# Optimization experiments

Measured on AMD Instinct MI355X. Metric: run time of the kernel, lower is better.

The kernel has to match this reference:

```python
import jax, jax.numpy as jnp
import numpy as np

B, T, D = 16, 4096, 256
CODEBOOK_SIZE = 1024
COMMITMENT = 1.0


def setup_inputs() -> dict:
    key = jax.random.key(0)
    kx, kc = jax.random.split(key)
    x = jax.random.normal(kx, (B, T, D), dtype=jnp.float32)
    codebook = jax.random.normal(kc, (CODEBOOK_SIZE, D), dtype=jnp.float32)
    return {"x": x, "codebook": codebook}


def reference(x, codebook):
    # x: [B, T, D] continuous latents; codebook: [K, D]
    flat = x.reshape(-1, x.shape[-1])  # [N, D]
    # does not affect argmin but is kept for faithfulness to torch.cdist-style math)
    x_sq = jnp.sum(flat * flat, axis=1, keepdims=True)            # [N, 1]
    c_sq = jnp.sum(codebook * codebook, axis=1)                   # [K]
    dist = x_sq - 2.0 * (flat @ codebook.T) + c_sq[None, :]       # [N, K]
    indices = jnp.argmin(dist, axis=1)                            # [N] int
    quantized = codebook[indices].reshape(x.shape)                # gather, [B, T, D]
    # commitment loss: encoder pulled toward (stopped) codes
    commit_loss = COMMITMENT * jnp.mean(
        (x - jax.lax.stop_gradient(quantized)) ** 2
    )
    # straight-through estimator
    out = x + jax.lax.stop_gradient(quantized - x)
    return out, indices.reshape(x.shape[:-1]), commit_loss
```

## Files before the change

kernel.cpp:

```cpp
#include <hip/hip_runtime.h>

#define N_TOK 65536
#define DIM   256
#define KCODE 1024

#define NTHREADS 256
#define TM 128
#define TN 128
#define BK 32
#define NCHUNK 8
#define NSTAGE 24

#define REFINE_EPS 0.125f
#define TIE_THETA 1.0e-4

#define WS_CSQ_OFF   16
#define WS_IDX_OFF   2048
#define WS_PAIRS_OFF (WS_IDX_OFF + N_TOK)
#define WS_CBPK_OFF  (WS_PAIRS_OFF + N_TOK * NCHUNK * 4)

typedef float f32x4  __attribute__((ext_vector_type(4)));
typedef short bf16x8 __attribute__((ext_vector_type(8)));
typedef short s16x8  __attribute__((ext_vector_type(8)));

__global__ void zero_loss_kernel(float* ws) {
    if (threadIdx.x == 0) ws[0] = 0.0f;
}

__global__ void rowsq_np_kernel(const float* __restrict__ m,
                                float* __restrict__ out, int rows) {
#pragma clang fp contract(off)
    int row = blockIdx.x * 16 + (threadIdx.x >> 4);
    int l   = threadIdx.x & 15;
    if (row >= rows) return;
    int h = l >> 3;
    int j = l & 7;
    const float* p = m + (size_t)row * DIM + h * 128 + j;
    float v = p[0];
    float r = v * v;
#pragma unroll
    for (int i = 1; i < 16; ++i) {
        float w  = p[i * 8];
        float w2 = w * w;
        r = r + w2;
    }
    float t = r + __shfl_xor(r, 1);
    t = t + __shfl_xor(t, 2);
    t = t + __shfl_xor(t, 4);
    t = t + __shfl_xor(t, 8);
    if (l == 0) out[row] = t;
}

__device__ __forceinline__ void ins2(float d, int idx,
                                     float& d1, int& i1, float& d2, int& i2) {
    if (d < d1 || (d == d1 && idx < i1)) {
        d2 = d1; i2 = i1; d1 = d; i1 = idx;
    } else if ((d < d2 || (d == d2 && idx < i2)) && idx != i1) {
        d2 = d; i2 = idx;
    }
}

__device__ __forceinline__ void f2bf_split(float v, short& hi, short& lo) {
    unsigned u = __float_as_uint(v);
    unsigned r = (u + 0x7fffu + ((u >> 16) & 1u)) >> 16;
    hi = (short)r;
    float hf = __uint_as_float(r << 16);
    float lf = v - hf;
    unsigned u2 = __float_as_uint(lf);
    unsigned r2 = (u2 + 0x7fffu + ((u2 >> 16) & 1u)) >> 16;
    lo = (short)r2;
}

__global__ void pack_tiles_kernel(const float* __restrict__ src,
                                  unsigned short* __restrict__ dst,
                                  int total) {
    int tid = blockIdx.x * blockDim.x + threadIdx.x;
    if (tid >= total) return;
    int s   = tid & 3;
    int r   = (tid >> 2) & 127;
    int kc  = (tid >> 9) & 7;
    int g   = tid >> 12;
    int oct = s ^ ((r >> 1) & 3);

    const float4* xr = reinterpret_cast<const float4*>(
        src + ((size_t)(g * 128 + r)) * DIM + kc * 32 + oct * 8);
    float4 v0 = xr[0];
    float4 v1 = xr[1];

    float f[8] = {v0.x, v0.y, v0.z, v0.w, v1.x, v1.y, v1.z, v1.w};
    s16x8 hv, lv;
#pragma unroll
    for (int i = 0; i < 8; ++i) {
        short h, l;
        f2bf_split(f[i], h, l);
        hv[i] = h; lv[i] = l;
    }
    size_t base_hi = (((size_t)(g * 16 + kc) * 128 + r) << 5) + s * 8;
    size_t base_lo = (((size_t)(g * 16 + 8 + kc) * 128 + r) << 5) + s * 8;
    *reinterpret_cast<s16x8*>(dst + base_hi) = hv;
    *reinterpret_cast<s16x8*>(dst + base_lo) = lv;
}

__device__ __forceinline__ void gload_lds16(const unsigned short* g, unsigned short* lds) {
    __builtin_amdgcn_global_load_lds(
        (const __attribute__((address_space(1))) unsigned int*)g,
        (__attribute__((address_space(3))) unsigned int*)lds, 16, 0, 0);
}

__launch_bounds__(NTHREADS, 5)
__global__ void vq_main_kernel(const unsigned short* __restrict__ xpk,
                               const unsigned short* __restrict__ cbpk,
                               const float* __restrict__ csq,
                               float4* __restrict__ pairs) {
    __shared__ __align__(16) unsigned short shbuf[2][2 * TM * BK];

    const int tid  = threadIdx.x;
    const int w    = tid >> 6;
    const int wy   = w >> 1;
    const int wx   = w & 1;
    const int lane = tid & 63;
    const int lm   = lane & 15;
    const int q    = lane >> 4;

    const int bx     = blockIdx.x;
    const int jj     = bx >> 3;
    const int grp    = (bx & 7) + ((jj >> 3) << 3);
    const int cchunk = jj & 7;
    const int tok0   = grp * TM;
    const int code0  = cchunk * TN;

    float cs_reg[4];
#pragma unroll
    for (int ni = 0; ni < 4; ++ni)
        cs_reg[ni] = csq[code0 + wx * 64 + ni * 16 + lm];

    f32x4 acc[4][4];
#pragma unroll
    for (int mi = 0; mi < 4; ++mi)
#pragma unroll
        for (int ni = 0; ni < 4; ++ni)
            acc[mi][ni] = (f32x4){0.f, 0.f, 0.f, 0.f};

    int offA[4], offB[4];
#pragma unroll
    for (int mi = 0; mi < 4; ++mi) {
        int r = wy * 64 + mi * 16 + lm;
        offA[mi] = r * BK + ((q ^ ((r >> 1) & 3)) * 8);
    }
#pragma unroll
    for (int ni = 0; ni < 4; ++ni) {
        int r = wx * 64 + ni * 16 + lm;
        offB[ni] = TM * BK + r * BK + ((q ^ ((r >> 1) & 3)) * 8);
    }

    const int lsrc = w * 1024 + lane * 8;
    auto stage = [&](int p, int s) {
        const int seg = s >> 3;
        const int kc  = s & 7;
        const int pa  = (seg == 2) ? 8 : 0;
        const int pb  = (seg == 1) ? 8 : 0;
        const unsigned short* ga = xpk  + (((size_t)(grp    * 16 + pa + kc)) << 12) + lsrc;
        const unsigned short* gb = cbpk + (((size_t)(cchunk * 16 + pb + kc)) << 12) + lsrc;
        unsigned short* At = &shbuf[p][w * 1024];
        unsigned short* Bt = &shbuf[p][TM * BK + w * 1024];
        gload_lds16(ga,       At);
        gload_lds16(ga + 512, At + 512);
        gload_lds16(gb,       Bt);
        gload_lds16(gb + 512, Bt + 512);
    };

    stage(0, 0);
    __syncthreads();

    int p = 0;
#pragma unroll 1
    for (int s = 0; s < NSTAGE; ++s) {
        if (s < NSTAGE - 1) stage(p ^ 1, s + 1);

        const unsigned short* buf = &shbuf[p][0];
        bf16x8 af[4], bf[4];
#pragma unroll
        for (int mi = 0; mi < 4; ++mi)
            af[mi] = *reinterpret_cast<const bf16x8*>(buf + offA[mi]);
#pragma unroll
        for (int ni = 0; ni < 4; ++ni)
            bf[ni] = *reinterpret_cast<const bf16x8*>(buf + offB[ni]);
#pragma unroll
        for (int mi = 0; mi < 4; ++mi)
#pragma unroll
            for (int ni = 0; ni < 4; ++ni)
                acc[mi][ni] = __builtin_amdgcn_mfma_f32_16x16x32_bf16(
                    af[mi], bf[ni], acc[mi][ni], 0, 0, 0);

        __syncthreads();
        p ^= 1;
    }

    float4 (*pairs_sh)[2] = reinterpret_cast<float4(*)[2]>(&shbuf[0][0]);

#pragma unroll
    for (int mi = 0; mi < 4; ++mi) {
#pragma unroll
        for (int r = 0; r < 4; ++r) {
            int row_local = wy * 64 + mi * 16 + q * 4 + r;
            float l1 = 3.4e38f, l2 = 3.4e38f;
            int   j1 = 0x7fffffff, j2 = 0x7fffffff;
#pragma unroll
            for (int ni = 0; ni < 4; ++ni) {
                float d = cs_reg[ni] - 2.0f * acc[mi][ni][r];
                ins2(d, code0 + wx * 64 + ni * 16 + lm, l1, j1, l2, j2);
            }
#pragma unroll
            for (int m = 1; m < 16; m <<= 1) {
                float o1 = __shfl_xor(l1, m);
                int   p1 = __shfl_xor(j1, m);
                float o2 = __shfl_xor(l2, m);
                int   p2 = __shfl_xor(j2, m);
                ins2(o1, p1, l1, j1, l2, j2);
                ins2(o2, p2, l1, j1, l2, j2);
            }
            if (lm == 0) {
                float4 pr;
                pr.x = l1; pr.y = l2;
                pr.z = __int_as_float(j1); pr.w = __int_as_float(j2);
                pairs_sh[row_local][wx] = pr;
            }
        }
    }
    __syncthreads();
    if (tid < TM) {
        float4 pa = pairs_sh[tid][0];
        float4 pb = pairs_sh[tid][1];
        float d1 = pa.x, d2 = pa.y;
        int   i1 = __float_as_int(pa.z), i2 = __float_as_int(pa.w);
        ins2(pb.x, __float_as_int(pb.z), d1, i1, d2, i2);
        ins2(pb.y, __float_as_int(pb.w), d1, i1, d2, i2);
        float4 pr;
        pr.x = d1; pr.y = d2;
        pr.z = __int_as_float(i1); pr.w = __int_as_float(i2);
        pairs[(size_t)(tok0 + tid) * NCHUNK + cchunk] = pr;
    }
}

__global__ void merge_refine_kernel(const float* __restrict__ x,
                                    const float* __restrict__ cb,
                                    const float4* __restrict__ pairs,
                                    int* __restrict__ idx_out) {
    int t = blockIdx.x * 256 + threadIdx.x;
    if (t >= N_TOK) return;
    float4 p0 = pairs[(size_t)t * NCHUNK];
    float d1 = p0.x, d2 = p0.y;
    int   i1 = __float_as_int(p0.z), i2 = __float_as_int(p0.w);
#pragma unroll
    for (int c = 1; c < NCHUNK; ++c) {
        float4 p = pairs[(size_t)t * NCHUNK + c];
        ins2(p.x, __float_as_int(p.z), d1, i1, d2, i2);
        ins2(p.y, __float_as_int(p.w), d1, i1, d2, i2);
    }

    int pick = i1;
    if (d2 - d1 < REFINE_EPS) {
        const float* xr = x + (size_t)t * DIM;
        const float* c1 = cb + (size_t)i1 * DIM;
        const float* c2 = cb + (size_t)i2 * DIM;
        double sA = 0.0, dA = 0.0, sB = 0.0, dB = 0.0;
        for (int k = 0; k < DIM; ++k) {
            double xv = (double)xr[k];
            double a  = (double)c1[k];
            double b  = (double)c2[k];
            sA += a * a; dA += xv * a;
            sB += b * b; dB += xv * b;
        }
        double DA  = sA - 2.0 * dA;
        double DB  = sB - 2.0 * dB;
        double gap = DB - DA;
        if (gap > TIE_THETA)       pick = i1;
        else if (gap < -TIE_THETA) pick = i2;
        else                       pick = (i1 < i2) ? i1 : i2;
    }
    idx_out[t] = pick;
}

__launch_bounds__(NTHREADS)
__global__ void output_kernel(const float* __restrict__ x,
                              const float* __restrict__ cb,
                              const int* __restrict__ idx,
                              float* __restrict__ out_q,
                              float* __restrict__ out_idx,
                              float* __restrict__ loss_ws) {
    __shared__ int   sh_idx[TM];
    __shared__ float wsum[4];
    const int tid  = threadIdx.x;
    const int tok0 = blockIdx.x * TM;

    if (tid < TM) sh_idx[tid] = idx[tok0 + tid];
    __syncthreads();

    float lsum = 0.0f;
    for (int t = 0; t < TM; ++t) {
        int code = sh_idx[t];
        float qv = cb[(size_t)code * DIM + tid];
        float xv = x[(size_t)(tok0 + t) * DIM + tid];
        out_q[(size_t)(tok0 + t) * DIM + tid] = xv + (qv - xv);
        float df = xv - qv;
        lsum = fmaf(df, df, lsum);
    }
    if (tid < TM) out_idx[tok0 + tid] = (float)sh_idx[tid];

#pragma unroll
    for (int off = 1; off < 64; off <<= 1) lsum += __shfl_xor(lsum, off);
    if ((tid & 63) == 0) wsum[tid >> 6] = lsum;
    __syncthreads();
    if (tid == 0) atomicAdd(loss_ws, (wsum[0] + wsum[1]) + (wsum[2] + wsum[3]));
}

__global__ void finalize_kernel(const float* ws, float* out_loss) {
    if (threadIdx.x == 0) out_loss[0] = ws[0] * (1.0f / 16777216.0f);
}

extern "C" void kernel_launch(void* const* d_in, const int* in_sizes, int n_in,
                              void* d_out, int out_size, void* d_ws, size_t ws_size,
                              hipStream_t stream) {
    const float* x  = (const float*)d_in[0];
    const float* cb = (const float*)d_in[1];

    float* out      = (float*)d_out;
    float* out_q    = out;
    float* out_idx  = out + (size_t)N_TOK * DIM;
    float* out_loss = out_idx + N_TOK;

    float*  ws    = (float*)d_ws;
    float*  csq   = ws + WS_CSQ_OFF;
    int*    idx   = (int*)(ws + WS_IDX_OFF);
    float4* pairs = (float4*)(ws + WS_PAIRS_OFF);
    unsigned short* cbpk = (unsigned short*)(ws + WS_CBPK_OFF);
    unsigned short* xpk  = (unsigned short*)out_q;

    zero_loss_kernel<<<1, 64, 0, stream>>>(ws);
    rowsq_np_kernel<<<KCODE / 16, 256, 0, stream>>>(cb, csq, KCODE);
    pack_tiles_kernel<<<(N_TOK * 32) / 256, 256, 0, stream>>>(x, xpk, N_TOK * 32);
    pack_tiles_kernel<<<(KCODE * 32) / 256, 256, 0, stream>>>(cb, cbpk, KCODE * 32);
    vq_main_kernel<<<(N_TOK / TM) * NCHUNK, NTHREADS, 0, stream>>>(xpk, cbpk, csq, pairs);
    merge_refine_kernel<<<N_TOK / 256, 256, 0, stream>>>(x, cb, pairs, idx);
    output_kernel<<<N_TOK / TM, NTHREADS, 0, stream>>>(x, cb, idx, out_q, out_idx, ws);
    finalize_kernel<<<1, 64, 0, stream>>>(ws, out_loss);
}
```

Measured before the change: 803.3 us.

## Load MFMA fragments directly from global memory instead of staging through LDS

The LDS double-buffered pipeline using global_load_lds is removed. Each wave now reads its bf16 fragments straight from the pre-packed global tiles, with the k-loop fully unrolled and no per-stage barriers. The pack layout drops the XOR swizzle, and the pairs buffer becomes chunk-major so merge reads are coalesced. This gives up LDS reuse across the waves, so each fragment is fetched from global or L2 by two waves, and the lower launch bound allows more registers per thread in exchange for occupancy.

```diff
diff --git a/kernel.cpp b/kernel.cpp
--- a/kernel.cpp
+++ b/kernel.cpp
@@ -7,7 +7,6 @@
 #define NTHREADS 256
 #define TM 128
 #define TN 128
-#define BK 32
 #define NCHUNK 8
 #define NSTAGE 24
 
@@ -80,10 +79,9 @@
     int r   = (tid >> 2) & 127;
     int kc  = (tid >> 9) & 7;
     int g   = tid >> 12;
-    int oct = s ^ ((r >> 1) & 3);
 
     const float4* xr = reinterpret_cast<const float4*>(
-        src + ((size_t)(g * 128 + r)) * DIM + kc * 32 + oct * 8);
+        src + ((size_t)(g * 128 + r)) * DIM + kc * 32 + s * 8);
     float4 v0 = xr[0];
     float4 v1 = xr[1];
 
@@ -101,18 +99,12 @@
     *reinterpret_cast<s16x8*>(dst + base_lo) = lv;
 }
 
-__device__ __forceinline__ void gload_lds16(const unsigned short* g, unsigned short* lds) {
-    __builtin_amdgcn_global_load_lds(
-        (const __attribute__((address_space(1))) unsigned int*)g,
-        (__attribute__((address_space(3))) unsigned int*)lds, 16, 0, 0);
-}
-
-__launch_bounds__(NTHREADS, 5)
+__launch_bounds__(NTHREADS, 2)
 __global__ void vq_main_kernel(const unsigned short* __restrict__ xpk,
                                const unsigned short* __restrict__ cbpk,
                                const float* __restrict__ csq,
                                float4* __restrict__ pairs) {
-    __shared__ __align__(16) unsigned short shbuf[2][2 * TM * BK];
+    __shared__ float4 pairs_sh[TM][2];
 
     const int tid  = threadIdx.x;
     const int w    = tid >> 6;
@@ -141,62 +133,35 @@
         for (int ni = 0; ni < 4; ++ni)
             acc[mi][ni] = (f32x4){0.f, 0.f, 0.f, 0.f};
 
-    int offA[4], offB[4];
-#pragma unroll
-    for (int mi = 0; mi < 4; ++mi) {
-        int r = wy * 64 + mi * 16 + lm;
-        offA[mi] = r * BK + ((q ^ ((r >> 1) & 3)) * 8);
-    }
-#pragma unroll
-    for (int ni = 0; ni < 4; ++ni) {
-        int r = wx * 64 + ni * 16 + lm;
-        offB[ni] = TM * BK + r * BK + ((q ^ ((r >> 1) & 3)) * 8);
-    }
-
-    const int lsrc = w * 1024 + lane * 8;
-    auto stage = [&](int p, int s) {
+    const unsigned short* abase =
+        xpk + ((size_t)grp << 16) + (wy * 64 + lm) * 32 + q * 8;
+    const unsigned short* bbase =
+        cbpk + ((size_t)cchunk << 16) + (wx * 64 + lm) * 32 + q * 8;
+
+#pragma unroll
+    for (int s = 0; s < NSTAGE; ++s) {
         const int seg = s >> 3;
         const int kc  = s & 7;
         const int pa  = (seg == 2) ? 8 : 0;
         const int pb  = (seg == 1) ? 8 : 0;
-        const unsigned short* ga = xpk  + (((size_t)(grp    * 16 + pa + kc)) << 12) + lsrc;
-        const unsigned short* gb = cbpk + (((size_t)(cchunk * 16 + pb + kc)) << 12) + lsrc;
-        unsigned short* At = &shbuf[p][w * 1024];
-        unsigned short* Bt = &shbuf[p][TM * BK + w * 1024];
-        gload_lds16(ga,       At);
-        gload_lds16(ga + 512, At + 512);
-        gload_lds16(gb,       Bt);
-        gload_lds16(gb + 512, Bt + 512);
-    };
-
-    stage(0, 0);
-    __syncthreads();
-
-    int p = 0;
-#pragma unroll 1
-    for (int s = 0; s < NSTAGE; ++s) {
-        if (s < NSTAGE - 1) stage(p ^ 1, s + 1);
-
-        const unsigned short* buf = &shbuf[p][0];
+        const unsigned short* ga = abase + (pa + kc) * 4096;
+        const unsigned short* gb = bbase + (pb + kc) * 4096;
+
         bf16x8 af[4], bf[4];
 #pragma unroll
         for (int mi = 0; mi < 4; ++mi)
-            af[mi] = *reinterpret_cast<const bf16x8*>(buf + offA[mi]);
+            af[mi] = *reinterpret_cast<const bf16x8*>(ga + mi * 512);
 #pragma unroll
         for (int ni = 0; ni < 4; ++ni)
-            bf[ni] = *reinterpret_cast<const bf16x8*>(buf + offB[ni]);
+            bf[ni] = *reinterpret_cast<const bf16x8*>(gb + ni * 512);
+
 #pragma unroll
         for (int mi = 0; mi < 4; ++mi)
 #pragma unroll
             for (int ni = 0; ni < 4; ++ni)
                 acc[mi][ni] = __builtin_amdgcn_mfma_f32_16x16x32_bf16(
                     af[mi], bf[ni], acc[mi][ni], 0, 0, 0);
-
-        __syncthreads();
-        p ^= 1;
-    }
-
-    float4 (*pairs_sh)[2] = reinterpret_cast<float4(*)[2]>(&shbuf[0][0]);
+    }
 
 #pragma unroll
     for (int mi = 0; mi < 4; ++mi) {
@@ -238,7 +203,7 @@
         float4 pr;
         pr.x = d1; pr.y = d2;
         pr.z = __int_as_float(i1); pr.w = __int_as_float(i2);
-        pairs[(size_t)(tok0 + tid) * NCHUNK + cchunk] = pr;
+        pairs[(size_t)cchunk * N_TOK + tok0 + tid] = pr;
     }
 }
 
@@ -248,12 +213,12 @@
                                     int* __restrict__ idx_out) {
     int t = blockIdx.x * 256 + threadIdx.x;
     if (t >= N_TOK) return;
-    float4 p0 = pairs[(size_t)t * NCHUNK];
+    float4 p0 = pairs[t];
     float d1 = p0.x, d2 = p0.y;
     int   i1 = __float_as_int(p0.z), i2 = __float_as_int(p0.w);
 #pragma unroll
     for (int c = 1; c < NCHUNK; ++c) {
-        float4 p = pairs[(size_t)t * NCHUNK + c];
+        float4 p = pairs[(size_t)c * N_TOK + t];
         ins2(p.x, __float_as_int(p.z), d1, i1, d2, i2);
         ins2(p.y, __float_as_int(p.w), d1, i1, d2, i2);
     }
```

After: 1.226 ms. 1.53x slower.
